# Performance work log

Measured on AMD Instinct MI355X. Metric: run time of the kernel, lower is better.

Reference implementation:

```python
import jax, jax.numpy as jnp
import numpy as np

LORA_DIM = 16          # hard-coded in module
LORA_TOKEN_INDEX = 1   # lora_dim*layer_sequence + 1 with layer_sequence=0
B, S, D, H = 4, 2048, 1024, 4096  # num_hiddens = 4*num_input (forced by view())


def setup_inputs() -> dict:
    key = jax.random.key(0)
    ks = jax.random.split(key, 6)
    x = jax.random.normal(ks[0], (B, S, D), dtype=jnp.float32)
    W1 = jax.random.normal(ks[1], (H, D), dtype=jnp.float32) * 0.02
    b1 = jnp.zeros((H,), dtype=jnp.float32)
    W2 = jax.random.normal(ks[2], (D, H), dtype=jnp.float32) * 0.02
    b2 = jnp.zeros((D,), dtype=jnp.float32)
    scale = jnp.asarray(0.001, dtype=jnp.float32)  # nn.Parameter(torch.tensor(0.001))
    return {"x": x, "W1": W1, "b1": b1, "W2": W2, "b2": b2, "scale": scale}


def reference(x, W1, b1, W2, b2, scale):
    Bx, Sx, Dx = x.shape
    Hx = W1.shape[0]  # = 4*Dx
    # 16 lora tokens starting at LORA_TOKEN_INDEX
    lt = jax.lax.dynamic_slice_in_dim(x, LORA_TOKEN_INDEX, LORA_DIM, axis=1)
    even = lt[:, ::2, :]  # (B, 8, D)
    odd = lt[:, 1::2, :]  # (B, 8, D)
    # per-sample low-rank weight updates:
    # result_multiplication[b,k] = outer(even[b,k], odd[b,k]) (D,D)
    # matrix1 = first 4 blocks stacked -> (B, 4D, D); matrix2 = last 4 reshaped -> (B, D, 4D)
    m1 = (even[:, :4, :, None] * odd[:, :4, None, :]).reshape(Bx, Hx, Dx)
    m2 = (even[:, 4:, :, None] * odd[:, 4:, None, :]).reshape(Bx, Dx, Hx)
    # x @ (W1 + scale*m1)^T + b1, fused without repeating W1 per batch
    h = jnp.einsum('bsd,hd->bsh', x, W1) + scale * jnp.einsum('bsd,bhd->bsh', x, m1) + b1
    h = jax.nn.gelu(h, approximate=False)  # torch nn.GELU default = exact erf
    out = jnp.einsum('bsh,oh->bso', h, W2) + scale * jnp.einsum('bsh,boh->bso', h, m2) + b2
    return out
```

## Files before the change

### kernel.cpp

```cpp
#include <hip/hip_runtime.h>
#include <cstdint>
#include <cstddef>

#define MROWS 8192
#define DDIM  1024
#define HDIM  4096

typedef __bf16 bf16x8 __attribute__((ext_vector_type(8)));
typedef float  f32x4  __attribute__((ext_vector_type(4)));

typedef __attribute__((address_space(1))) void* as1_vp;
typedef __attribute__((address_space(3))) void* as3_vp;

__device__ __forceinline__ unsigned short f2bf(float f) {
  unsigned int u = __builtin_bit_cast(unsigned int, f);
  u += 0x7fffu + ((u >> 16) & 1u);
  return (unsigned short)(u >> 16);
}
__device__ __forceinline__ float bf2f(unsigned short h) {
  return __builtin_bit_cast(float, (unsigned int)h << 16);
}

__device__ __forceinline__ float fast_gelu(float x) {
  float x3 = x * x * x;
  float z = 0.7978845608028654f * x + 0.03567740814f * x3;
  float e = __builtin_amdgcn_exp2f(z * 2.8853900817779268f);
  float t = 1.0f - 2.0f * __builtin_amdgcn_rcpf(e + 1.0f);
  return 0.5f * x * (1.0f + t);
}

__device__ __forceinline__ void gld_lds16(const unsigned short* g, unsigned short* lds) {
  __builtin_amdgcn_global_load_lds((as1_vp)(uintptr_t)g, (as3_vp)lds, 16, 0, 0);
}

#define VMW(n) asm volatile("s_waitcnt vmcnt(" #n ")" ::: "memory")
#define LKW()  asm volatile("s_waitcnt lgkmcnt(0)" ::: "memory")
#define BAR()  asm volatile("s_barrier" ::: "memory")

__global__ __launch_bounds__(256) void pre_kernel(
    const float* __restrict__ x, const float* __restrict__ w1,
    const float* __restrict__ w2, unsigned short* __restrict__ xb,
    unsigned short* __restrict__ w1b, unsigned short* __restrict__ w2b,
    float* __restrict__ p1) {
  if (blockIdx.x < 8192) {
    int i = blockIdx.x * 256 + threadIdx.x;
    const float* src; unsigned short* dst; int off;
    if (i < 1048576) { src = w1; dst = w1b; off = i; }
    else             { src = w2; dst = w2b; off = i - 1048576; }
    float4 v = ((const float4*)src)[off];
    ushort4 o;
    o.x = f2bf(v.x); o.y = f2bf(v.y); o.z = f2bf(v.z); o.w = f2bf(v.w);
    ((ushort4*)dst)[off] = o;
    return;
  }
  const int bid = blockIdx.x - 8192;
  const int wave = threadIdx.x >> 6, lane = threadIdx.x & 63;
  const int m = bid * 4 + wave;
  const int b = m >> 11;
  const float4* xrow4 = (const float4*)(x + (size_t)m * DDIM);
  const float4* od4   = (const float4*)(x + ((size_t)b * 2048 + 2) * DDIM);
  ushort4* xbrow4 = (ushort4*)(xb + (size_t)m * DDIM);
  float a0 = 0.f, a1 = 0.f, a2 = 0.f, a3 = 0.f;
#pragma unroll
  for (int it = 0; it < 4; ++it) {
    int g = it * 64 + lane;
    float4 v = xrow4[g];
    ushort4 o; o.x = f2bf(v.x); o.y = f2bf(v.y); o.z = f2bf(v.z); o.w = f2bf(v.w);
    xbrow4[g] = o;
    float4 o0 = od4[g];
    float4 o1 = od4[512 + g];
    float4 o2 = od4[1024 + g];
    float4 o3 = od4[1536 + g];
    a0 += v.x * o0.x + v.y * o0.y + v.z * o0.z + v.w * o0.w;
    a1 += v.x * o1.x + v.y * o1.y + v.z * o1.z + v.w * o1.w;
    a2 += v.x * o2.x + v.y * o2.y + v.z * o2.z + v.w * o2.w;
    a3 += v.x * o3.x + v.y * o3.y + v.z * o3.z + v.w * o3.w;
  }
#pragma unroll
  for (int off = 32; off > 0; off >>= 1) {
    a0 += __shfl_down(a0, off);
    a1 += __shfl_down(a1, off);
    a2 += __shfl_down(a2, off);
    a3 += __shfl_down(a3, off);
  }
  if (lane == 0) {
    float4 r; r.x = a0; r.y = a1; r.z = a2; r.w = a3;
    ((float4*)p1)[m] = r;
  }
}

__global__ __launch_bounds__(512, 2) void gemm1_kernel(
    const unsigned short* __restrict__ xb, const unsigned short* __restrict__ w1b,
    const float* __restrict__ x, const float* __restrict__ b1,
    const float* __restrict__ p1, const float* __restrict__ scale_p,
    unsigned short* __restrict__ hact) {
  __shared__ __align__(16) unsigned short As[4 * 256 * 32];
  __shared__ __align__(16) unsigned short Bs[4 * 256 * 32];

  const int id = blockIdx.x;
  const int xcd = id & 7, w = id >> 3;
  const int m0 = (xcd * 4 + (w & 3)) * 256;
  const int n0 = (w >> 2) * 256;

  const int tid  = threadIdx.x;
  const int wave = tid >> 6, lane = tid & 63;
  const int quad = lane >> 4, l16 = lane & 15;
  const int wm2  = wave >> 2;
  const int wn2  = wave & 3;

  const unsigned short *gA0, *gA1, *gB0, *gB1;
  {
    int idx = tid;
    int r = idx >> 2, sl = idx & 3, c = (sl - (r >> 1)) & 3;
    gA0 = xb  + (size_t)(m0 + r) * DDIM + c * 8;
    gB0 = w1b + (size_t)(n0 + r) * DDIM + c * 8;
    idx = 512 + tid;
    r = idx >> 2; sl = idx & 3; c = (sl - (r >> 1)) & 3;
    gA1 = xb  + (size_t)(m0 + r) * DDIM + c * 8;
    gB1 = w1b + (size_t)(n0 + r) * DDIM + c * 8;
  }
  const int ldsOff0 = (wave * 64) * 8;
  const int ldsOff1 = (512 + wave * 64) * 8;

#define STAGE1(tt, sb) do {                                   \
    const int _k = (tt) * 32;                                 \
    unsigned short* _a = &As[(sb) * 8192];                    \
    unsigned short* _b = &Bs[(sb) * 8192];                    \
    gld_lds16(gA0 + _k, _a + ldsOff0);                        \
    gld_lds16(gA1 + _k, _a + ldsOff1);                        \
    gld_lds16(gB0 + _k, _b + ldsOff0);                        \
    gld_lds16(gB1 + _k, _b + ldsOff1);                        \
  } while (0)

  f32x4 acc[8][4];
  const f32x4 z = {0.f, 0.f, 0.f, 0.f};
#pragma unroll
  for (int i = 0; i < 8; ++i)
#pragma unroll
    for (int j = 0; j < 4; ++j) acc[i][j] = z;

  bf16x8 a[8], b[4];

  auto RA = [&](int nb) {
    const unsigned short* Ab = As + nb * 8192;
    const unsigned short* Bb = Bs + nb * 8192;
#pragma unroll
    for (int j = 0; j < 4; ++j) {
      const int rb = wn2 * 64 + j * 16 + l16;
      b[j] = *(const bf16x8*)(Bb + rb * 32 + ((quad + (rb >> 1)) & 3) * 8);
    }
#pragma unroll
    for (int i = 0; i < 4; ++i) {
      const int ra = wm2 * 128 + i * 16 + l16;
      a[i] = *(const bf16x8*)(Ab + ra * 32 + ((quad + (ra >> 1)) & 3) * 8);
    }
  };
  auto RB = [&](int cb) {
    const unsigned short* Ab = As + cb * 8192;
#pragma unroll
    for (int i = 4; i < 8; ++i) {
      const int ra = wm2 * 128 + i * 16 + l16;
      a[i] = *(const bf16x8*)(Ab + ra * 32 + ((quad + (ra >> 1)) & 3) * 8);
    }
  };
  auto MFA = [&]() {
    __builtin_amdgcn_s_setprio(1);
#pragma unroll
    for (int i = 0; i < 4; ++i)
#pragma unroll
      for (int j = 0; j < 4; ++j)
        acc[i][j] = __builtin_amdgcn_mfma_f32_16x16x32_bf16(a[i], b[j], acc[i][j], 0, 0, 0);
    __builtin_amdgcn_s_setprio(0);
  };
  auto MFB = [&]() {
    __builtin_amdgcn_s_setprio(1);
#pragma unroll
    for (int i = 4; i < 8; ++i)
#pragma unroll
      for (int j = 0; j < 4; ++j)
        acc[i][j] = __builtin_amdgcn_mfma_f32_16x16x32_bf16(a[i], b[j], acc[i][j], 0, 0, 0);
    __builtin_amdgcn_s_setprio(0);
  };

#define G1BODY(cb, sb, nb, tt) do {   \
    LKW(); MFA();                     \
    RB(cb);                           \
    STAGE1((tt) + 3, sb);             \
    VMW(8);                           \
    LKW(); MFB();                     \
    BAR();                            \
    RA(nb);                           \
  } while (0)

  STAGE1(0, 0);
  STAGE1(1, 1);
  STAGE1(2, 2);
  VMW(8); BAR();
  RA(0);

#pragma unroll 1
  for (int t = 0; t < 28; t += 4) {
    G1BODY(0, 3, 1, t + 0);
    G1BODY(1, 0, 2, t + 1);
    G1BODY(2, 1, 3, t + 2);
    G1BODY(3, 2, 0, t + 3);
  }
  LKW(); MFA(); RB(0); STAGE1(31, 3); VMW(8); LKW(); MFB(); BAR(); RA(1);
  LKW(); MFA(); RB(1); VMW(4); LKW(); MFB(); BAR(); RA(2);
  LKW(); MFA(); RB(2); VMW(0); LKW(); MFB(); BAR(); RA(3);
  LKW(); MFA(); RB(3); LKW(); MFB();

  const float sc = scale_p[0];
  const int bidx = m0 >> 11;
  const int i1 = (n0 + wn2 * 64) >> 10;
  const float* exrow = x + ((size_t)(bidx * 2048 + 1 + 2 * i1)) * DDIM;

  float exv[4], b1v[4]; int nn[4];
#pragma unroll
  for (int j = 0; j < 4; ++j) {
    nn[j]  = n0 + wn2 * 64 + j * 16 + l16;
    exv[j] = exrow[nn[j] & 1023];
    b1v[j] = b1[nn[j]];
  }
#pragma unroll
  for (int i = 0; i < 8; ++i) {
#pragma unroll
    for (int r = 0; r < 4; ++r) {
      const int m = m0 + wm2 * 128 + i * 16 + quad * 4 + r;
      const float pv = p1[(size_t)m * 4 + i1] * sc;
#pragma unroll
      for (int j = 0; j < 4; ++j) {
        float v = acc[i][j][r] + b1v[j] + pv * exv[j];
        hact[(size_t)m * HDIM + nn[j]] = f2bf(fast_gelu(v));
      }
    }
  }
#undef G1BODY
#undef STAGE1
}

__global__ __launch_bounds__(512, 2) void gemm2_kernel(
    const unsigned short* __restrict__ hact, const unsigned short* __restrict__ w2b,
    const float* __restrict__ x, const float* __restrict__ b2,
    const float* __restrict__ scale_p, float* __restrict__ out) {
  __shared__ __align__(16) unsigned short As[3 * 256 * 64];
  __shared__ __align__(16) unsigned short Bs[3 * 128 * 64];
  __shared__ __align__(16) unsigned short od_lds[1024];
  __shared__ __align__(16) float p2s[256 * 4];

  const int id = blockIdx.x;
  const int xcd = id & 7, w = id >> 3;
  const int m0 = (xcd * 4 + (w & 3)) * 256;
  const int n0 = (w >> 2) * 128;
  const int tid = threadIdx.x;
  const int wave = tid >> 6, lane = tid & 63, quad = lane >> 4, l16 = lane & 15;
  const int wmq = (wave >> 1) * 64;
  const int wnq = (wave & 1) * 64;
  const bool hi = (wave & 1);
  const int bidx = m0 >> 11;
  const int i2 = n0 >> 8;

  if (tid < 256) {
    const float4* src = (const float4*)(x + ((size_t)(bidx * 2048 + 10 + 2 * i2)) * DDIM);
    float4 v = src[tid];
    ushort4 o; o.x = f2bf(v.x); o.y = f2bf(v.y); o.z = f2bf(v.z); o.w = f2bf(v.w);
    ((ushort4*)od_lds)[tid] = o;
  }
  LKW();

  f32x4 acc[4][4];
  const f32x4 z = {0.f, 0.f, 0.f, 0.f};
#pragma unroll
  for (int i = 0; i < 4; ++i)
#pragma unroll
    for (int j = 0; j < 4; ++j) acc[i][j] = z;
  f32x4 pacc[2] = {z, z};
  const bf16x8 zer8 = __builtin_bit_cast(bf16x8, z);

  const unsigned short *gA[4], *gB[2];
#pragma unroll
  for (int s = 0; s < 4; ++s) {
    int idx = (wave * 4 + s) * 64 + lane;
    int r = idx >> 3, sl = idx & 7, c = (sl - r) & 7;
    gA[s] = hact + (size_t)(m0 + r) * HDIM + c * 8;
  }
#pragma unroll
  for (int s = 0; s < 2; ++s) {
    int idx = (wave * 2 + s) * 64 + lane;
    int r = idx >> 3, sl = idx & 7, c = (sl - r) & 7;
    gB[s] = w2b + (size_t)(n0 + r) * HDIM + c * 8;
  }

#define STAGE2(tt, sb) do {                                   \
    const int _k = (tt) * 64;                                 \
    unsigned short* _a = &As[(sb) * 16384];                   \
    unsigned short* _b = &Bs[(sb) * 8192];                    \
    gld_lds16(gA[0] + _k, _a + (wave * 4 + 0) * 512);         \
    gld_lds16(gA[1] + _k, _a + (wave * 4 + 1) * 512);         \
    gld_lds16(gA[2] + _k, _a + (wave * 4 + 2) * 512);         \
    gld_lds16(gA[3] + _k, _a + (wave * 4 + 3) * 512);         \
    gld_lds16(gB[0] + _k, _b + (wave * 2 + 0) * 512);         \
    gld_lds16(gB[1] + _k, _b + (wave * 2 + 1) * 512);         \
  } while (0)

  bf16x8 a[4], b[4], odv;

  auto RPH = [&](int nb, int kk, int odk) {
    const unsigned short* Ab = As + nb * 16384;
    const unsigned short* Bb = Bs + nb * 8192;
    odv = *(const bf16x8*)(od_lds + odk + kk + quad * 8);
    const int cb = (kk >> 3) + quad;
#pragma unroll
    for (int j = 0; j < 4; ++j) {
      const int rb = wnq + j * 16 + l16;
      b[j] = *(const bf16x8*)(Bb + rb * 64 + ((cb + rb) & 7) * 8);
    }
#pragma unroll
    for (int i = 0; i < 4; ++i) {
      const int ra = wmq + i * 16 + l16;
      a[i] = *(const bf16x8*)(Ab + ra * 64 + ((cb + ra) & 7) * 8);
    }
  };
  auto MPH = [&]() {
    bf16x8 bod = (l16 == 0) ? odv : zer8;
    bf16x8 pa0 = hi ? a[2] : a[0];
    bf16x8 pa1 = hi ? a[3] : a[1];
    pacc[0] = __builtin_amdgcn_mfma_f32_16x16x32_bf16(pa0, bod, pacc[0], 0, 0, 0);
    pacc[1] = __builtin_amdgcn_mfma_f32_16x16x32_bf16(pa1, bod, pacc[1], 0, 0, 0);
    __builtin_amdgcn_s_setprio(1);
#pragma unroll
    for (int i = 0; i < 4; ++i)
#pragma unroll
      for (int j = 0; j < 4; ++j)
        acc[i][j] = __builtin_amdgcn_mfma_f32_16x16x32_bf16(a[i], b[j], acc[i][j], 0, 0, 0);
    __builtin_amdgcn_s_setprio(0);
  };
  auto flush_p2 = [&](int seg) {
    const int ibase = hi ? 2 : 0;
    if (l16 == 0) {
#pragma unroll
      for (int ip = 0; ip < 2; ++ip)
#pragma unroll
        for (int e = 0; e < 4; ++e)
          p2s[(wmq + (ibase + ip) * 16 + quad * 4 + e) * 4 + seg] = pacc[ip][e];
    }
    pacc[0] = z; pacc[1] = z;
  };

#define G2BODY(cb, sb, nb, tt) do {                 \
    LKW(); MPH();                                   \
    RPH(cb, 32, ((tt) * 64) & 1023);                \
    STAGE2((tt) + 2, sb);                           \
    VMW(6);                                         \
    LKW(); MPH();                                   \
    if (((tt) & 15) == 15) flush_p2((tt) >> 4);     \
    BAR();                                          \
    RPH(nb, 0, (((tt) + 1) * 64) & 1023);           \
  } while (0)

  STAGE2(0, 0);
  STAGE2(1, 1);
  VMW(6); BAR();
  RPH(0, 0, 0);

#pragma unroll 1
  for (int t = 0; t < 60; t += 3) {
    G2BODY(0, 2, 1, t + 0);
    G2BODY(1, 0, 2, t + 1);
    G2BODY(2, 1, 0, t + 2);
  }
  LKW(); MPH(); RPH(0, 32, (60 * 64) & 1023); STAGE2(62, 2); VMW(6);
  LKW(); MPH(); BAR(); RPH(1, 0, (61 * 64) & 1023);
  LKW(); MPH(); RPH(1, 32, (61 * 64) & 1023); STAGE2(63, 0); VMW(6);
  LKW(); MPH(); BAR(); RPH(2, 0, (62 * 64) & 1023);
  LKW(); MPH(); RPH(2, 32, (62 * 64) & 1023); VMW(0);
  LKW(); MPH(); BAR(); RPH(0, 0, (63 * 64) & 1023);
  LKW(); MPH(); RPH(0, 32, (63 * 64) & 1023);
  LKW(); MPH();
  flush_p2(3);
  LKW();
  BAR();

  const float sc = scale_p[0];
  const float* evrow = x + ((size_t)(bidx * 2048 + 9 + 2 * i2)) * DDIM;

  float4 ev[4]; float b2v[4]; int nn[4];
#pragma unroll
  for (int j = 0; j < 4; ++j) {
    nn[j] = n0 + wnq + j * 16 + l16;
    ev[j]  = *(const float4*)(evrow + 4 * (nn[j] & 255));
    b2v[j] = b2[nn[j]];
  }
#pragma unroll
  for (int i = 0; i < 4; ++i) {
#pragma unroll
    for (int r = 0; r < 4; ++r) {
      const int mloc = wmq + i * 16 + quad * 4 + r;
      const int m = m0 + mloc;
      const float4 pv = *(const float4*)(p2s + mloc * 4);
#pragma unroll
      for (int j = 0; j < 4; ++j) {
        float lora = ev[j].x * pv.x + ev[j].y * pv.y + ev[j].z * pv.z + ev[j].w * pv.w;
        out[(size_t)m * DDIM + nn[j]] = acc[i][j][r] + b2v[j] + sc * lora;
      }
    }
  }
#undef G2BODY
#undef STAGE2
}

extern "C" void kernel_launch(void* const* d_in, const int* in_sizes, int n_in,
                              void* d_out, int out_size, void* d_ws, size_t ws_size,
                              hipStream_t stream) {
  const float* x     = (const float*)d_in[0];
  const float* W1    = (const float*)d_in[1];
  const float* b1    = (const float*)d_in[2];
  const float* W2    = (const float*)d_in[3];
  const float* b2    = (const float*)d_in[4];
  const float* scale = (const float*)d_in[5];
  float* out = (float*)d_out;

  char* ws = (char*)d_ws;
  unsigned short* xb   = (unsigned short*)(ws);
  unsigned short* w1b  = (unsigned short*)(ws + 16777216);
  unsigned short* w2b  = (unsigned short*)(ws + 25165824);
  unsigned short* hact = (unsigned short*)(ws + 33554432);
  float*          p1   = (float*)(ws + 100663296);

  pre_kernel<<<dim3(10240), dim3(256), 0, stream>>>(x, W1, W2, xb, w1b, w2b, p1);
  gemm1_kernel<<<dim3(512), dim3(512), 0, stream>>>(xb, w1b, x, b1, p1, scale, hact);
  gemm2_kernel<<<dim3(256), dim3(512), 0, stream>>>(hact, w2b, x, b2, scale, out);
}
```

Baseline: 255.9 us.

## Double-buffer LDS fragment registers and overlap reads with MFMAs in both GEMMs

Both GEMM main loops are rebuilt so the LDS fragment reads for the next phase are issued while the current phase's MFMAs run. This uses ping-pong register sets, partial lgkmcnt waits and sched_barrier fences in place of full lgkmcnt(0) waits. GEMM1's LDS staging drops from four buffers to three, with a prefetch distance of two and a new loop unroll, which frees shared memory. The intent is to hide LDS latency behind matrix math. The cost is a shallower global prefetch and more live VGPRs, which could cause spills at the 512-thread, 2-block launch bounds.

```diff
diff --git a/kernel.cpp b/kernel.cpp
--- a/kernel.cpp
+++ b/kernel.cpp
@@ -33,9 +33,10 @@
   __builtin_amdgcn_global_load_lds((as1_vp)(uintptr_t)g, (as3_vp)lds, 16, 0, 0);
 }
 
-#define VMW(n) asm volatile("s_waitcnt vmcnt(" #n ")" ::: "memory")
-#define LKW()  asm volatile("s_waitcnt lgkmcnt(0)" ::: "memory")
-#define BAR()  asm volatile("s_barrier" ::: "memory")
+#define VMW(n)  asm volatile("s_waitcnt vmcnt(" #n ")" ::: "memory")
+#define LKWN(n) asm volatile("s_waitcnt lgkmcnt(" #n ")" ::: "memory")
+#define BAR()   asm volatile("s_barrier" ::: "memory")
+#define SB0()   __builtin_amdgcn_sched_barrier(0)
 
 __global__ __launch_bounds__(256) void pre_kernel(
     const float* __restrict__ x, const float* __restrict__ w1,
@@ -94,8 +95,8 @@
     const float* __restrict__ x, const float* __restrict__ b1,
     const float* __restrict__ p1, const float* __restrict__ scale_p,
     unsigned short* __restrict__ hact) {
-  __shared__ __align__(16) unsigned short As[4 * 256 * 32];
-  __shared__ __align__(16) unsigned short Bs[4 * 256 * 32];
+  __shared__ __align__(16) unsigned short As[3 * 256 * 32];
+  __shared__ __align__(16) unsigned short Bs[3 * 256 * 32];
 
   const int id = blockIdx.x;
   const int xcd = id & 7, w = id >> 3;
@@ -139,76 +140,85 @@
 #pragma unroll
     for (int j = 0; j < 4; ++j) acc[i][j] = z;
 
-  bf16x8 a[8], b[4];
-
-  auto RA = [&](int nb) {
-    const unsigned short* Ab = As + nb * 8192;
-    const unsigned short* Bb = Bs + nb * 8192;
+  bf16x8 a03A[4], a47A[4], bA[4];
+  bf16x8 a03B[4], a47B[4], bB[4];
+
+  auto rd_ph0 = [&](const unsigned short* Ab, const unsigned short* Bb,
+                    bf16x8 (&aa)[4], bf16x8 (&bb)[4]) {
 #pragma unroll
     for (int j = 0; j < 4; ++j) {
       const int rb = wn2 * 64 + j * 16 + l16;
-      b[j] = *(const bf16x8*)(Bb + rb * 32 + ((quad + (rb >> 1)) & 3) * 8);
+      bb[j] = *(const bf16x8*)(Bb + rb * 32 + ((quad + (rb >> 1)) & 3) * 8);
     }
 #pragma unroll
     for (int i = 0; i < 4; ++i) {
       const int ra = wm2 * 128 + i * 16 + l16;
-      a[i] = *(const bf16x8*)(Ab + ra * 32 + ((quad + (ra >> 1)) & 3) * 8);
-    }
-  };
-  auto RB = [&](int cb) {
-    const unsigned short* Ab = As + cb * 8192;
-#pragma unroll
-    for (int i = 4; i < 8; ++i) {
-      const int ra = wm2 * 128 + i * 16 + l16;
-      a[i] = *(const bf16x8*)(Ab + ra * 32 + ((quad + (ra >> 1)) & 3) * 8);
-    }
-  };
-  auto MFA = [&]() {
+      aa[i] = *(const bf16x8*)(Ab + ra * 32 + ((quad + (ra >> 1)) & 3) * 8);
+    }
+  };
+  auto rd_ph1 = [&](const unsigned short* Ab, bf16x8 (&aa)[4]) {
+#pragma unroll
+    for (int i = 0; i < 4; ++i) {
+      const int ra = wm2 * 128 + (i + 4) * 16 + l16;
+      aa[i] = *(const bf16x8*)(Ab + ra * 32 + ((quad + (ra >> 1)) & 3) * 8);
+    }
+  };
+  auto mf_ph0 = [&](bf16x8 (&aa)[4], bf16x8 (&bb)[4]) {
     __builtin_amdgcn_s_setprio(1);
 #pragma unroll
     for (int i = 0; i < 4; ++i)
 #pragma unroll
       for (int j = 0; j < 4; ++j)
-        acc[i][j] = __builtin_amdgcn_mfma_f32_16x16x32_bf16(a[i], b[j], acc[i][j], 0, 0, 0);
+        acc[i][j] = __builtin_amdgcn_mfma_f32_16x16x32_bf16(aa[i], bb[j], acc[i][j], 0, 0, 0);
     __builtin_amdgcn_s_setprio(0);
   };
-  auto MFB = [&]() {
+  auto mf_ph1 = [&](bf16x8 (&aa)[4], bf16x8 (&bb)[4]) {
     __builtin_amdgcn_s_setprio(1);
 #pragma unroll
-    for (int i = 4; i < 8; ++i)
+    for (int i = 0; i < 4; ++i)
 #pragma unroll
       for (int j = 0; j < 4; ++j)
-        acc[i][j] = __builtin_amdgcn_mfma_f32_16x16x32_bf16(a[i], b[j], acc[i][j], 0, 0, 0);
+        acc[4 + i][j] = __builtin_amdgcn_mfma_f32_16x16x32_bf16(aa[i], bb[j], acc[4 + i][j], 0, 0, 0);
     __builtin_amdgcn_s_setprio(0);
   };
 
-#define G1BODY(cb, sb, nb, tt) do {   \
-    LKW(); MFA();                     \
-    RB(cb);                           \
-    STAGE1((tt) + 3, sb);             \
-    VMW(8);                           \
-    LKW(); MFB();                     \
-    BAR();                            \
-    RA(nb);                           \
+#define G1BODY(tt, CB, NB, SB, CUR, NXT) do {                        \
+    STAGE1((tt) + 2, SB);                                            \
+    VMW(4); BAR();                                                   \
+    rd_ph1(&As[(CB) * 8192], a47##CUR);                              \
+    LKWN(4); SB0();                                                  \
+    mf_ph0(a03##CUR, b##CUR);                                        \
+    rd_ph0(&As[(NB) * 8192], &Bs[(NB) * 8192], a03##NXT, b##NXT);    \
+    LKWN(8); SB0(); BAR();                                           \
+    mf_ph1(a47##CUR, b##CUR);                                        \
   } while (0)
 
   STAGE1(0, 0);
   STAGE1(1, 1);
-  STAGE1(2, 2);
-  VMW(8); BAR();
-  RA(0);
+  VMW(4); BAR();
+  rd_ph0(&As[0], &Bs[0], a03A, bA);
 
 #pragma unroll 1
-  for (int t = 0; t < 28; t += 4) {
-    G1BODY(0, 3, 1, t + 0);
-    G1BODY(1, 0, 2, t + 1);
-    G1BODY(2, 1, 3, t + 2);
-    G1BODY(3, 2, 0, t + 3);
-  }
-  LKW(); MFA(); RB(0); STAGE1(31, 3); VMW(8); LKW(); MFB(); BAR(); RA(1);
-  LKW(); MFA(); RB(1); VMW(4); LKW(); MFB(); BAR(); RA(2);
-  LKW(); MFA(); RB(2); VMW(0); LKW(); MFB(); BAR(); RA(3);
-  LKW(); MFA(); RB(3); LKW(); MFB();
+  for (int t = 0; t < 30; t += 6) {
+    G1BODY(t + 0, 0, 1, 2, A, B);
+    G1BODY(t + 1, 1, 2, 0, B, A);
+    G1BODY(t + 2, 2, 0, 1, A, B);
+    G1BODY(t + 3, 0, 1, 2, B, A);
+    G1BODY(t + 4, 1, 2, 0, A, B);
+    G1BODY(t + 5, 2, 0, 1, B, A);
+  }
+  VMW(0); BAR();
+  rd_ph1(&As[0], a47A);
+  LKWN(4); SB0();
+  mf_ph0(a03A, bA);
+  rd_ph0(&As[1 * 8192], &Bs[1 * 8192], a03B, bB);
+  LKWN(8); SB0(); BAR();
+  mf_ph1(a47A, bA);
+  rd_ph1(&As[1 * 8192], a47B);
+  LKWN(4); SB0();
+  mf_ph0(a03B, bB);
+  LKWN(0); SB0();
+  mf_ph1(a47B, bB);
 
   const float sc = scale_p[0];
   const int bidx = m0 >> 11;
@@ -266,7 +276,7 @@
     ushort4 o; o.x = f2bf(v.x); o.y = f2bf(v.y); o.z = f2bf(v.z); o.w = f2bf(v.w);
     ((ushort4*)od_lds)[tid] = o;
   }
-  LKW();
+  LKWN(0);
 
   f32x4 acc[4][4];
   const f32x4 z = {0.f, 0.f, 0.f, 0.f};
@@ -303,28 +313,28 @@
     gld_lds16(gB[1] + _k, _b + (wave * 2 + 1) * 512);         \
   } while (0)
 
-  bf16x8 a[4], b[4], odv;
-
-  auto RPH = [&](int nb, int kk, int odk) {
-    const unsigned short* Ab = As + nb * 16384;
-    const unsigned short* Bb = Bs + nb * 8192;
-    odv = *(const bf16x8*)(od_lds + odk + kk + quad * 8);
+  bf16x8 aK0[4], bK0[4], odv0;
+  bf16x8 aK1[4], bK1[4], odv1;
+
+  auto rd_ph = [&](const unsigned short* Ab, const unsigned short* Bb,
+                   int kk, int odk, bf16x8 (&aa)[4], bf16x8 (&bb)[4], bf16x8& ov) {
+    ov = *(const bf16x8*)(od_lds + odk + kk + quad * 8);
     const int cb = (kk >> 3) + quad;
 #pragma unroll
     for (int j = 0; j < 4; ++j) {
       const int rb = wnq + j * 16 + l16;
-      b[j] = *(const bf16x8*)(Bb + rb * 64 + ((cb + rb) & 7) * 8);
+      bb[j] = *(const bf16x8*)(Bb + rb * 64 + ((cb + rb) & 7) * 8);
     }
 #pragma unroll
     for (int i = 0; i < 4; ++i) {
       const int ra = wmq + i * 16 + l16;
-      a[i] = *(const bf16x8*)(Ab + ra * 64 + ((cb + ra) & 7) * 8);
-    }
-  };
-  auto MPH = [&]() {
-    bf16x8 bod = (l16 == 0) ? odv : zer8;
-    bf16x8 pa0 = hi ? a[2] : a[0];
-    bf16x8 pa1 = hi ? a[3] : a[1];
+      aa[i] = *(const bf16x8*)(Ab + ra * 64 + ((cb + ra) & 7) * 8);
+    }
+  };
+  auto mf_ph = [&](bf16x8 (&aa)[4], bf16x8 (&bb)[4], bf16x8& ov) {
+    bf16x8 bod = (l16 == 0) ? ov : zer8;
+    bf16x8 pa0 = hi ? aa[2] : aa[0];
+    bf16x8 pa1 = hi ? aa[3] : aa[1];
     pacc[0] = __builtin_amdgcn_mfma_f32_16x16x32_bf16(pa0, bod, pacc[0], 0, 0, 0);
     pacc[1] = __builtin_amdgcn_mfma_f32_16x16x32_bf16(pa1, bod, pacc[1], 0, 0, 0);
     __builtin_amdgcn_s_setprio(1);
@@ -332,7 +342,7 @@
     for (int i = 0; i < 4; ++i)
 #pragma unroll
       for (int j = 0; j < 4; ++j)
-        acc[i][j] = __builtin_amdgcn_mfma_f32_16x16x32_bf16(a[i], b[j], acc[i][j], 0, 0, 0);
+        acc[i][j] = __builtin_amdgcn_mfma_f32_16x16x32_bf16(aa[i], bb[j], acc[i][j], 0, 0, 0);
     __builtin_amdgcn_s_setprio(0);
   };
   auto flush_p2 = [&](int seg) {
@@ -347,38 +357,47 @@
     pacc[0] = z; pacc[1] = z;
   };
 
-#define G2BODY(cb, sb, nb, tt) do {                 \
-    LKW(); MPH();                                   \
-    RPH(cb, 32, ((tt) * 64) & 1023);                \
-    STAGE2((tt) + 2, sb);                           \
-    VMW(6);                                         \
-    LKW(); MPH();                                   \
-    if (((tt) & 15) == 15) flush_p2((tt) >> 4);     \
-    BAR();                                          \
-    RPH(nb, 0, (((tt) + 1) * 64) & 1023);           \
+#define G2BODY(tt, CB, NB, SB) do {                                         \
+    STAGE2((tt) + 2, SB);                                                   \
+    VMW(6); BAR();                                                          \
+    rd_ph(&As[(CB) * 16384], &Bs[(CB) * 8192], 32, ((tt) * 64) & 1023,      \
+          aK1, bK1, odv1);                                                  \
+    LKWN(9); SB0();                                                         \
+    mf_ph(aK0, bK0, odv0);                                                  \
+    rd_ph(&As[(NB) * 16384], &Bs[(NB) * 8192], 0, (((tt) + 1) * 64) & 1023, \
+          aK0, bK0, odv0);                                                  \
+    LKWN(9); SB0(); BAR();                                                  \
+    mf_ph(aK1, bK1, odv1);                                                  \
+    if (((tt) & 15) == 15) flush_p2((tt) >> 4);                             \
   } while (0)
 
   STAGE2(0, 0);
   STAGE2(1, 1);
   VMW(6); BAR();
-  RPH(0, 0, 0);
+  rd_ph(&As[0], &Bs[0], 0, 0, aK0, bK0, odv0);
 
 #pragma unroll 1
   for (int t = 0; t < 60; t += 3) {
-    G2BODY(0, 2, 1, t + 0);
-    G2BODY(1, 0, 2, t + 1);
-    G2BODY(2, 1, 0, t + 2);
-  }
-  LKW(); MPH(); RPH(0, 32, (60 * 64) & 1023); STAGE2(62, 2); VMW(6);
-  LKW(); MPH(); BAR(); RPH(1, 0, (61 * 64) & 1023);
-  LKW(); MPH(); RPH(1, 32, (61 * 64) & 1023); STAGE2(63, 0); VMW(6);
-  LKW(); MPH(); BAR(); RPH(2, 0, (62 * 64) & 1023);
-  LKW(); MPH(); RPH(2, 32, (62 * 64) & 1023); VMW(0);
-  LKW(); MPH(); BAR(); RPH(0, 0, (63 * 64) & 1023);
-  LKW(); MPH(); RPH(0, 32, (63 * 64) & 1023);
-  LKW(); MPH();
+    G2BODY(t + 0, 0, 1, 2);
+    G2BODY(t + 1, 1, 2, 0);
+    G2BODY(t + 2, 2, 0, 1);
+  }
+  G2BODY(60, 0, 1, 2);
+  G2BODY(61, 1, 2, 0);
+  VMW(0); BAR();
+  rd_ph(&As[2 * 16384], &Bs[2 * 8192], 32, 896, aK1, bK1, odv1);
+  LKWN(9); SB0();
+  mf_ph(aK0, bK0, odv0);
+  rd_ph(&As[0], &Bs[0], 0, 960, aK0, bK0, odv0);
+  LKWN(9); SB0(); BAR();
+  mf_ph(aK1, bK1, odv1);
+  rd_ph(&As[0], &Bs[0], 32, 960, aK1, bK1, odv1);
+  LKWN(9); SB0();
+  mf_ph(aK0, bK0, odv0);
+  LKWN(0); SB0();
+  mf_ph(aK1, bK1, odv1);
   flush_p2(3);
-  LKW();
+  LKWN(0);
   BAR();
 
   const float sc = scale_p[0];
```

Result: slower. 275.6 us (+7.7%).
